# Performance work log

Hardware: AMD Instinct MI355X
Metric: run time of the kernel (lower is better)

Reference implementation:

```python
import jax, jax.numpy as jnp
import numpy as np

B, MAX_OBJS, D = 8, 12, 512
NUM_OBJ, NUM_ACT, NUM_TRS = 37, 6, 3
EMBED = 128
NUM_AA = 100
NUM_CLASSES = 300
ACT_THRES = 0.5
K = MAX_OBJS * NUM_ACT            # 72 candidate (object, action) slots
FINAL_DIM = 2 * (D + 2 * EMBED)   # 1536
# All ordered pairs (i, j), i != j, in lexicographic order. itertools.permutations
# over a sorted index subset is exactly the valid-masked subsequence of this list.
_pairs = np.array([(i, j) for i in range(K) for j in range(K) if i != j], dtype=np.int64)
PAIR_I = jnp.asarray(_pairs[:, 0])
PAIR_J = jnp.asarray(_pairs[:, 1])
P = _pairs.shape[0]               # K*(K-1) = 5112 (static max num pairs)


def setup_inputs() -> dict:
    key = jax.random.key(0)
    ks = jax.random.split(key, 12)
    inp = jax.random.normal(ks[0], (B, MAX_OBJS, D), jnp.float32)
    objmask = jnp.ones((B, MAX_OBJS), jnp.float32)
    # -1 marks 'no composite-action target' for that (obj, act) slot
    AAidxs_tgts = jax.random.randint(ks[1], (B, K), -1, NUM_AA)
    TR_tgts = jax.random.uniform(ks[2], (B, K, K, NUM_TRS), jnp.float32)
    obj_act_lookup = jax.random.randint(ks[3], (NUM_OBJ, NUM_ACT), 0, NUM_AA)
    aa_aa_tr_lookup = jax.random.randint(ks[4], (NUM_AA, NUM_AA, NUM_TRS), 0, NUM_CLASSES)
    s = lambda k, shape: (jax.random.normal(k, shape, jnp.float32) * 0.02)
    return {
        'inp': inp, 'objmask': objmask,
        'TR_tgts': TR_tgts,
        'W_obj': s(ks[5], (NUM_OBJ, D)), 'b_obj': jnp.zeros((NUM_OBJ,), jnp.float32),
        'W_act': s(ks[6], (NUM_ACT, D)), 'b_act': jnp.zeros((NUM_ACT,), jnp.float32),
        'W_tr': s(ks[7], (NUM_TRS, FINAL_DIM)), 'b_tr': jnp.zeros((NUM_TRS,), jnp.float32),
        'W_ne': s(ks[8], (NUM_CLASSES, D)), 'b_ne': jnp.zeros((NUM_CLASSES,), jnp.float32),
        'obj_emb': s(ks[9], (NUM_OBJ, EMBED)), 'act_emb': s(ks[10], (NUM_ACT, EMBED)),
        'AAidxs_tgts': AAidxs_tgts,
        'obj_act_lookup': obj_act_lookup,
        'aa_aa_tr_lookup': aa_aa_tr_lookup,
    }


def reference(inp, objmask, TR_tgts, W_obj, b_obj, W_act, b_act, W_tr, b_tr,
              W_ne, b_ne, obj_emb, act_emb, AAidxs_tgts, obj_act_lookup,
              aa_aa_tr_lookup):
    # training branch (is_eval=False); obj_act_lookup only used in eval branch
    exp_objmask = jnp.repeat(objmask, NUM_ACT, axis=1)                # [B,K]
    masked = inp * objmask[:, :, None]
    pooled = masked.sum(axis=1) / objmask.sum(axis=1, keepdims=True)  # [B,D]
    non_exist_out = pooled @ W_ne.T + b_ne                            # [B,C]
    obj_out = inp @ W_obj.T + b_obj                                   # [B,MO,NO]
    act_out = inp @ W_act.T + b_act                                   # [B,MO,NA]

    posb_action_idxs = jnp.tile(jnp.arange(NUM_ACT), (B, MAX_OBJS))   # [B,K]
    pred_obj_idxs = jnp.repeat(jnp.argmax(obj_out, axis=-1), NUM_ACT, axis=1)  # [B,K]
    posb_inputs = jnp.repeat(inp, NUM_ACT, axis=1)                    # [B,K,D]

    pred_act = (jax.nn.sigmoid(act_out.reshape(B, K)) > ACT_THRES).astype(jnp.float32)
    pred_act = pred_act * exp_objmask
    selected = (pred_act == 1.0) & (AAidxs_tgts != -1)                # [B,K]
    aaidx = jnp.where(selected, AAidxs_tgts, -1)

    posb_obj_emb = obj_emb[pred_obj_idxs]                             # [B,K,E]
    posb_act_emb = act_emb[posb_action_idxs]                          # [B,K,E]
    comp = jnp.concatenate([posb_inputs, posb_obj_emb, posb_act_emb], axis=-1)  # [B,K,FINAL/2]

    # pack valid pairs to the front (stable sort preserves lexicographic order,
    # matching itertools.permutations over the sorted selected index set)
    valid = selected[:, PAIR_I] & selected[:, PAIR_J]                 # [B,P]
    order = jnp.argsort(~valid, axis=1, stable=True)                  # [B,P]
    valid_p = jnp.take_along_axis(valid, order, axis=1)
    i_p = jnp.take_along_axis(jnp.broadcast_to(PAIR_I, (B, P)), order, axis=1)
    j_p = jnp.take_along_axis(jnp.broadcast_to(PAIR_J, (B, P)), order, axis=1)
    b_ix = jnp.arange(B)[:, None]

    pair_out = jnp.where(valid_p[..., None],
                         jnp.concatenate([comp[b_ix, i_p], comp[b_ix, j_p]], axis=-1),
                         -1.0)                                        # [B,P,FINAL_DIM]
    pair_logits = pair_out @ W_tr.T + b_tr                            # [B,P,3]

    aai = aaidx[b_ix, i_p]
    aaj = aaidx[b_ix, j_p]
    ca = aa_aa_tr_lookup[jnp.maximum(aai, 0), jnp.maximum(aaj, 0)]    # [B,P,3]
    ca = jnp.where(valid_p[..., None], ca, -1)
    tr_targets = jnp.where(valid_p[..., None], TR_tgts[b_ix, i_p, j_p], -1.0)

    # diag(logit) @ one_hot(ca) then masked max over pairs == segment max per class
    flat_logit = pair_logits.reshape(B, P * NUM_TRS)
    flat_ca = ca.reshape(B, P * NUM_TRS)
    flat_valid = jnp.repeat(valid_p, NUM_TRS, axis=1)
    seg = jnp.where(flat_valid, flat_ca, NUM_CLASSES)                 # dump invalid to extra segment
    seg_max = jax.vmap(lambda l, s: jax.ops.segment_max(l, s, num_segments=NUM_CLASSES + 1))(
        flat_logit, seg)[:, :NUM_CLASSES]                             # [B,C]
    counts = jax.vmap(lambda s: jax.ops.segment_sum(jnp.ones_like(s), s, num_segments=NUM_CLASSES + 1))(
        seg)[:, :NUM_CLASSES]
    exist = counts > 0
    final_outputs = jnp.where(exist, seg_max, non_exist_out)          # [B,C]

    return final_outputs, pair_logits, tr_targets, act_out, obj_out
```

## Files before the change

kernel.cpp:

```cpp
#include <hip/hip_runtime.h>
#include <hip/hip_bf16.h>

#define Bn    8
#define MO    12
#define Dd    512
#define NOBJ  37
#define NACT  6
#define NTRS  3
#define EMB   128
#define NAA   100
#define NCLS  300
#define Kk    72
#define Pp    5112
#define HALF  768
#define FD    1536

#define OUT_FINAL 0
#define OUT_PLOG  (Bn*NCLS)
#define OUT_TTGT  (OUT_PLOG + Bn*Pp*NTRS)
#define OUT_ACT   (OUT_TTGT + Bn*Pp*NTRS)
#define OUT_OBJ   (OUT_ACT + Bn*Kk)

#define WS_LINP 0
#define WS_EO   (WS_LINP + Bn*MO*6)
#define WS_EA   (WS_EO + NOBJ*6)
#define WS_INV  (WS_EA + NACT*6)
#define WS_NE   (WS_INV + 6)
#define WS_SEG  (WS_NE + Bn*NCLS)
#define WS_PRED (WS_SEG + Bn*NCLS)
#define WS_SEL  (WS_PRED + Bn*MO)
#define WS_AAI  (WS_SEL + Bn*Kk)

__device__ __forceinline__ unsigned fmap(float f) {
  unsigned u = __float_as_uint(f);
  return (u & 0x80000000u) ? ~u : (u | 0x80000000u);
}
__device__ __forceinline__ float funmap(unsigned u) {
  return __uint_as_float((u & 0x80000000u) ? (u & 0x7fffffffu) : ~u);
}

__device__ __forceinline__ float wreduce(float v) {
#pragma unroll
  for (int off = 32; off > 0; off >>= 1) v += __shfl_xor(v, off, 64);
  return v;
}

__device__ __forceinline__ float dotW(const float* __restrict__ wrow,
                                      float4 x0, float4 x1, int lane) {
  const float4* w4 = (const float4*)wrow;
  float4 w0 = w4[lane], w1 = w4[lane + 64];
  float s0 = fmaf(w0.x, x0.x, fmaf(w0.y, x0.y, fmaf(w0.z, x0.z, w0.w * x0.w)));
  float s1 = fmaf(w1.x, x1.x, fmaf(w1.y, x1.y, fmaf(w1.z, x1.z, w1.w * x1.w)));
  return wreduce(s0 + s1);
}

__device__ __forceinline__ float dot512_wave(const float* __restrict__ a,
                                             const float* __restrict__ b, int lane) {
  const float4* b4 = (const float4*)b;
  return dotW(a, b4[lane], b4[lane + 64], lane);
}

__device__ __forceinline__ float dot128_wave(const float* __restrict__ a,
                                             const float* __restrict__ b, int lane) {
  const float2* a2 = (const float2*)a;
  const float2* b2 = (const float2*)b;
  float2 x = a2[lane], y = b2[lane];
  return wreduce(fmaf(x.x, y.x, x.y * y.y));
}

#define W_TOBJ  (Bn*MO)
#define W_TACT  (W_TOBJ + Bn*MO)
#define W_TLINP (W_TACT + Bn*MO*6)
#define W_TEO   (W_TLINP + NOBJ*6)
#define W_TEA   (W_TEO + NACT*6)
#define W_TINV  (W_TEA + NTRS)
#define W_TNE   (W_TINV + Bn*NCLS)
#define W_TOT   (W_TNE + 38)

__global__ __launch_bounds__(256) void k1(
    const float* __restrict__ inp, const float* __restrict__ objmask,
    const float* __restrict__ W_obj, const float* __restrict__ b_obj,
    const float* __restrict__ W_act, const float* __restrict__ b_act,
    const float* __restrict__ W_tr, const float* __restrict__ b_tr,
    const float* __restrict__ W_ne, const float* __restrict__ b_ne,
    const float* __restrict__ obj_emb, const float* __restrict__ act_emb,
    const int* __restrict__ AA,
    float* __restrict__ out, float* __restrict__ ws)
{
  int gt = blockIdx.x * 256 + threadIdx.x;
  int w = gt >> 6, lane = gt & 63;

  if (w < W_TOBJ) {
    int b = w / MO, o = w % MO;
    const float4* x4 = (const float4*)(inp + (b*MO + o)*Dd);
    float4 x0 = x4[lane], x1 = x4[lane + 64];
    float myval = 0.f, best = 0.f;
    int bi = 0;
    for (int c = 0; c < NOBJ; ++c) {
      float s = dotW(W_obj + c*Dd, x0, x1, lane) + b_obj[c];
      if (lane == c) myval = s;
      if (c == 0 || s > best) { best = s; bi = c; }
    }
    if (lane < NOBJ) out[OUT_OBJ + (b*MO + o)*NOBJ + lane] = myval;
    if (lane == 0) ((int*)ws)[WS_PRED + b*MO + o] = bi;
  } else if (w < W_TACT) {
    int r = w - W_TOBJ, b = r / MO, o = r % MO;
    const float4* x4 = (const float4*)(inp + (b*MO + o)*Dd);
    float4 x0 = x4[lane], x1 = x4[lane + 64];
    float myv = 0.f;
    for (int a = 0; a < NACT; ++a) {
      float s = dotW(W_act + a*Dd, x0, x1, lane) + b_act[a];
      if (lane == a) myv = s;
    }
    if (lane < NACT) {
      int k = o*NACT + lane;
      out[OUT_ACT + b*Kk + k] = myv;
      int aa = AA[b*Kk + k];
      int sel = (myv > 0.f) && (objmask[b*MO + o] == 1.0f) && (aa != -1);
      ((int*)ws)[WS_SEL + b*Kk + k] = sel;
      ((int*)ws)[WS_AAI + b*Kk + k] = sel ? aa : -1;
    }
  } else if (w < W_TLINP) {
    int r = w - W_TACT, b = r / (MO*6), r2 = r % (MO*6), o = r2 / 6, th = r2 % 6;
    int t = th >> 1, h = th & 1;
    float v = dot512_wave(W_tr + t*FD + h*HALF, inp + (b*MO + o)*Dd, lane);
    if (!lane) ws[WS_LINP + (b*MO + o)*6 + th] = v;
  } else if (w < W_TEO) {
    int r = w - W_TLINP, oc = r / 6, th = r % 6, t = th >> 1, h = th & 1;
    float v = dot128_wave(W_tr + t*FD + h*HALF + Dd, obj_emb + oc*EMB, lane);
    if (!lane) ws[WS_EO + oc*6 + th] = v;
  } else if (w < W_TEA) {
    int r = w - W_TEO, a = r / 6, th = r % 6, t = th >> 1, h = th & 1;
    float v = dot128_wave(W_tr + t*FD + h*HALF + Dd + EMB, act_emb + a*EMB, lane);
    if (!lane) ws[WS_EA + a*6 + th] = v;
  } else if (w < W_TINV) {
    int t = w - W_TEA;
    const float4* w4 = (const float4*)(W_tr + t*FD);
    float s = 0.f;
#pragma unroll
    for (int i = 0; i < 6; ++i) { float4 x = w4[lane + 64*i]; s += x.x + x.y + x.z + x.w; }
    s = wreduce(s);
    if (!lane) ws[WS_INV + t] = b_tr[t] - s;
  } else if (w < W_TNE) {
    int r = w - W_TINV, b = r / NCLS, c = r % NCLS;
    const float4* i4 = (const float4*)inp;
    float msum = 0.f;
    float4 p0 = make_float4(0.f, 0.f, 0.f, 0.f), p1 = p0;
#pragma unroll
    for (int o = 0; o < MO; ++o) {
      float m = objmask[b*MO + o];
      msum += m;
      float4 v0 = i4[(b*MO + o)*128 + lane];
      float4 v1 = i4[(b*MO + o)*128 + lane + 64];
      p0.x = fmaf(m, v0.x, p0.x); p0.y = fmaf(m, v0.y, p0.y);
      p0.z = fmaf(m, v0.z, p0.z); p0.w = fmaf(m, v0.w, p0.w);
      p1.x = fmaf(m, v1.x, p1.x); p1.y = fmaf(m, v1.y, p1.y);
      p1.z = fmaf(m, v1.z, p1.z); p1.w = fmaf(m, v1.w, p1.w);
    }
    float v = dotW(W_ne + c*Dd, p0, p1, lane) / msum + b_ne[c];
    if (!lane) ws[WS_NE + b*NCLS + c] = v;
  } else if (w < W_TOT) {
    int idx = (w - W_TNE)*64 + lane;
    if (idx < Bn*NCLS) ((unsigned*)ws)[WS_SEG + idx] = 0u;
  }
}

#define NSLICE 20

__global__ __launch_bounds__(256) void k2(
    const float* __restrict__ TRt, const float* __restrict__ b_tr,
    const int* __restrict__ aalut,
    float* __restrict__ out, float* __restrict__ ws)
{
  __shared__ float s_L[Kk*6];
  __shared__ float s_inv[NTRS];
  __shared__ int s_sel[Kk], s_aa[Kk], s_C[Kk], s_T;

  int b = blockIdx.x / NSLICE, slice = blockIdx.x % NSLICE;
  int tid = threadIdx.x;

  if (tid < Kk) {
    s_sel[tid] = ((const int*)ws)[WS_SEL + b*Kk + tid];
    s_aa[tid]  = ((const int*)ws)[WS_AAI + b*Kk + tid];
  } else if (tid < Kk + NTRS) {
    s_inv[tid - Kk] = ws[WS_INV + (tid - Kk)];
  }
  for (int m = tid; m < Kk*6; m += 256) {
    int k = m / 6, th = m % 6, t = th >> 1, h = th & 1;
    int o = k / NACT, a = k % NACT;
    int po = ((const int*)ws)[WS_PRED + b*MO + o];
    float v = ws[WS_LINP + (b*MO + o)*6 + th] + ws[WS_EO + po*6 + th] + ws[WS_EA + a*6 + th];
    if (h == 0) v += b_tr[t];
    s_L[m] = v;
  }
  __syncthreads();
  if (tid == 0) {
    int c = 0;
    for (int k = 0; k < Kk; ++k) { s_C[k] = c; c += s_sel[k]; }
    s_T = c;
  }
  __syncthreads();

  int T = s_T, Vtot = T*(T-1);
  int q = slice*256 + tid;
  if (q < Pp) {
    float* plog = out + OUT_PLOG + (size_t)b*Pp*NTRS;
    float* ttgt = out + OUT_TTGT + (size_t)b*Pp*NTRS;
    int i = q / (Kk-1);
    int jj = q - i*(Kk-1);
    int j = jj + (jj >= i ? 1 : 0);
    int si = s_sel[i], sj = s_sel[j];
    int vb = s_C[i]*(T-1) + (si ? (s_C[j] - (i < j ? 1 : 0)) : 0);
    bool valid = si && sj;
    int pos = valid ? vb : (Vtot + q - vb);
    float l0, l1, l2;
    if (valid) {
      l0 = s_L[i*6+0] + s_L[j*6+1];
      l1 = s_L[i*6+2] + s_L[j*6+3];
      l2 = s_L[i*6+4] + s_L[j*6+5];
    } else { l0 = s_inv[0]; l1 = s_inv[1]; l2 = s_inv[2]; }
    int ob = pos*3;
    plog[ob+0] = l0; plog[ob+1] = l1; plog[ob+2] = l2;
    if (valid) {
      const float* tr = TRt + (((size_t)b*Kk + i)*Kk + j)*NTRS;
      ttgt[ob+0] = tr[0]; ttgt[ob+1] = tr[1]; ttgt[ob+2] = tr[2];
      int base = (s_aa[i]*NAA + s_aa[j])*NTRS;
      unsigned* seg = (unsigned*)ws + WS_SEG + b*NCLS;
      atomicMax(&seg[aalut[base+0]], fmap(l0));
      atomicMax(&seg[aalut[base+1]], fmap(l1));
      atomicMax(&seg[aalut[base+2]], fmap(l2));
    } else {
      ttgt[ob+0] = -1.f; ttgt[ob+1] = -1.f; ttgt[ob+2] = -1.f;
    }
  }
}

__global__ __launch_bounds__(320) void k3(float* __restrict__ out,
                                          const float* __restrict__ ws)
{
  int b = blockIdx.x, c = threadIdx.x;
  if (c < NCLS) {
    unsigned u = ((const unsigned*)ws)[WS_SEG + b*NCLS + c];
    out[OUT_FINAL + b*NCLS + c] = u ? funmap(u) : ws[WS_NE + b*NCLS + c];
  }
}

extern "C" void kernel_launch(void* const* d_in, const int* in_sizes, int n_in,
                              void* d_out, int out_size, void* d_ws, size_t ws_size,
                              hipStream_t stream) {
  (void)in_sizes; (void)n_in; (void)ws_size; (void)out_size;
  const float* inp      = (const float*)d_in[0];
  const float* objmask  = (const float*)d_in[1];
  const float* TRt      = (const float*)d_in[2];
  const float* W_obj    = (const float*)d_in[3];
  const float* b_obj    = (const float*)d_in[4];
  const float* W_act    = (const float*)d_in[5];
  const float* b_act    = (const float*)d_in[6];
  const float* W_tr     = (const float*)d_in[7];
  const float* b_tr     = (const float*)d_in[8];
  const float* W_ne     = (const float*)d_in[9];
  const float* b_ne     = (const float*)d_in[10];
  const float* obj_emb  = (const float*)d_in[11];
  const float* act_emb  = (const float*)d_in[12];
  const int*   AA       = (const int*)d_in[13];
  const int*   aalut    = (const int*)d_in[15];
  float* out = (float*)d_out;
  float* ws  = (float*)d_ws;

  hipLaunchKernelGGL(k1, dim3((W_TOT + 3) / 4), dim3(256), 0, stream,
                     inp, objmask, W_obj, b_obj, W_act, b_act, W_tr, b_tr,
                     W_ne, b_ne, obj_emb, act_emb, AA, out, ws);
  hipLaunchKernelGGL(k2, dim3(Bn * NSLICE), dim3(256), 0, stream,
                     TRt, b_tr, aalut, out, ws);
  hipLaunchKernelGGL(k3, dim3(Bn), dim3(320), 0, stream, out, ws);
}
```

Before: 102.2 us.

## Spread obj/act logits across waves and fold finalize kernel into k2 via last-block counter

```diff
diff --git a/kernel.cpp b/kernel.cpp
--- a/kernel.cpp
+++ b/kernel.cpp
@@ -25,11 +25,12 @@
 #define WS_EO   (WS_LINP + Bn*MO*6)
 #define WS_EA   (WS_EO + NOBJ*6)
 #define WS_INV  (WS_EA + NACT*6)
-#define WS_NE   (WS_INV + 6)
-#define WS_SEG  (WS_NE + Bn*NCLS)
-#define WS_PRED (WS_SEG + Bn*NCLS)
-#define WS_SEL  (WS_PRED + Bn*MO)
-#define WS_AAI  (WS_SEL + Bn*Kk)
+#define WS_NE   840
+#define WS_OBJ  (WS_NE + Bn*NCLS)
+#define WS_ACT  (WS_OBJ + Bn*MO*NOBJ)
+#define WS_SEG  (WS_ACT + Bn*Kk)
+#define WS_CNT  (WS_SEG + Bn*NCLS)
+#define NZERO   (Bn*NCLS + Bn)
 
 __device__ __forceinline__ unsigned fmap(float f) {
   unsigned u = __float_as_uint(f);
@@ -68,14 +69,14 @@
   return wreduce(fmaf(x.x, y.x, x.y * y.y));
 }
 
-#define W_TOBJ  (Bn*MO)
-#define W_TACT  (W_TOBJ + Bn*MO)
-#define W_TLINP (W_TACT + Bn*MO*6)
-#define W_TEO   (W_TLINP + NOBJ*6)
-#define W_TEA   (W_TEO + NACT*6)
-#define W_TINV  (W_TEA + NTRS)
-#define W_TNE   (W_TINV + Bn*NCLS)
-#define W_TOT   (W_TNE + 38)
+#define W_OBJ_E  (Bn*MO*NOBJ)
+#define W_ACT_E  (W_OBJ_E + Bn*Kk)
+#define W_LINP_E (W_ACT_E + Bn*MO*6)
+#define W_EO_E   (W_LINP_E + NOBJ*6)
+#define W_EA_E   (W_EO_E + NACT*6)
+#define W_INV_E  (W_EA_E + NTRS)
+#define W_NE_E   (W_INV_E + Bn*NCLS)
+#define W_TOT    (W_NE_E + 38)
 
 __global__ __launch_bounds__(256) void k1(
     const float* __restrict__ inp, const float* __restrict__ objmask,
@@ -84,65 +85,44 @@
     const float* __restrict__ W_tr, const float* __restrict__ b_tr,
     const float* __restrict__ W_ne, const float* __restrict__ b_ne,
     const float* __restrict__ obj_emb, const float* __restrict__ act_emb,
-    const int* __restrict__ AA,
     float* __restrict__ out, float* __restrict__ ws)
 {
   int gt = blockIdx.x * 256 + threadIdx.x;
   int w = gt >> 6, lane = gt & 63;
 
-  if (w < W_TOBJ) {
-    int b = w / MO, o = w % MO;
-    const float4* x4 = (const float4*)(inp + (b*MO + o)*Dd);
-    float4 x0 = x4[lane], x1 = x4[lane + 64];
-    float myval = 0.f, best = 0.f;
-    int bi = 0;
-    for (int c = 0; c < NOBJ; ++c) {
-      float s = dotW(W_obj + c*Dd, x0, x1, lane) + b_obj[c];
-      if (lane == c) myval = s;
-      if (c == 0 || s > best) { best = s; bi = c; }
-    }
-    if (lane < NOBJ) out[OUT_OBJ + (b*MO + o)*NOBJ + lane] = myval;
-    if (lane == 0) ((int*)ws)[WS_PRED + b*MO + o] = bi;
-  } else if (w < W_TACT) {
-    int r = w - W_TOBJ, b = r / MO, o = r % MO;
-    const float4* x4 = (const float4*)(inp + (b*MO + o)*Dd);
-    float4 x0 = x4[lane], x1 = x4[lane + 64];
-    float myv = 0.f;
-    for (int a = 0; a < NACT; ++a) {
-      float s = dotW(W_act + a*Dd, x0, x1, lane) + b_act[a];
-      if (lane == a) myv = s;
-    }
-    if (lane < NACT) {
-      int k = o*NACT + lane;
-      out[OUT_ACT + b*Kk + k] = myv;
-      int aa = AA[b*Kk + k];
-      int sel = (myv > 0.f) && (objmask[b*MO + o] == 1.0f) && (aa != -1);
-      ((int*)ws)[WS_SEL + b*Kk + k] = sel;
-      ((int*)ws)[WS_AAI + b*Kk + k] = sel ? aa : -1;
-    }
-  } else if (w < W_TLINP) {
-    int r = w - W_TACT, b = r / (MO*6), r2 = r % (MO*6), o = r2 / 6, th = r2 % 6;
+  if (w < W_OBJ_E) {
+    int b = w / (MO*NOBJ), r = w % (MO*NOBJ), o = r / NOBJ, c = r % NOBJ;
+    float v = dot512_wave(W_obj + c*Dd, inp + (b*MO + o)*Dd, lane) + b_obj[c];
+    if (!lane) { out[OUT_OBJ + (b*MO + o)*NOBJ + c] = v; ws[WS_OBJ + (b*MO + o)*NOBJ + c] = v; }
+  } else if (w < W_ACT_E) {
+    int r = w - W_OBJ_E, b = r / Kk, k = r % Kk, o = k / NACT, a = k % NACT;
+    float v = dot512_wave(W_act + a*Dd, inp + (b*MO + o)*Dd, lane) + b_act[a];
+    if (!lane) { out[OUT_ACT + b*Kk + k] = v; ws[WS_ACT + b*Kk + k] = v; }
+  } else if (w < W_LINP_E) {
+    int r = w - W_ACT_E, b = r / (MO*6), r2 = r % (MO*6), o = r2 / 6, th = r2 % 6;
     int t = th >> 1, h = th & 1;
     float v = dot512_wave(W_tr + t*FD + h*HALF, inp + (b*MO + o)*Dd, lane);
     if (!lane) ws[WS_LINP + (b*MO + o)*6 + th] = v;
-  } else if (w < W_TEO) {
-    int r = w - W_TLINP, oc = r / 6, th = r % 6, t = th >> 1, h = th & 1;
+  } else if (w < W_EO_E) {
+    int r = w - W_LINP_E, oc = r / 6, th = r % 6, t = th >> 1, h = th & 1;
     float v = dot128_wave(W_tr + t*FD + h*HALF + Dd, obj_emb + oc*EMB, lane);
     if (!lane) ws[WS_EO + oc*6 + th] = v;
-  } else if (w < W_TEA) {
-    int r = w - W_TEO, a = r / 6, th = r % 6, t = th >> 1, h = th & 1;
-    float v = dot128_wave(W_tr + t*FD + h*HALF + Dd + EMB, act_emb + a*EMB, lane);
-    if (!lane) ws[WS_EA + a*6 + th] = v;
-  } else if (w < W_TINV) {
-    int t = w - W_TEA;
-    const float4* w4 = (const float4*)(W_tr + t*FD);
-    float s = 0.f;
+  } else if (w < W_INV_E) {
+    if (w < W_EA_E) {
+      int r = w - W_EO_E, a = r / 6, th = r % 6, t = th >> 1, h = th & 1;
+      float v = dot128_wave(W_tr + t*FD + h*HALF + Dd + EMB, act_emb + a*EMB, lane);
+      if (!lane) ws[WS_EA + a*6 + th] = v;
+    } else {
+      int t = w - W_EA_E;
+      const float4* w4 = (const float4*)(W_tr + t*FD);
+      float s = 0.f;
 #pragma unroll
-    for (int i = 0; i < 6; ++i) { float4 x = w4[lane + 64*i]; s += x.x + x.y + x.z + x.w; }
-    s = wreduce(s);
-    if (!lane) ws[WS_INV + t] = b_tr[t] - s;
-  } else if (w < W_TNE) {
-    int r = w - W_TINV, b = r / NCLS, c = r % NCLS;
+      for (int i = 0; i < 6; ++i) { float4 x = w4[lane + 64*i]; s += x.x + x.y + x.z + x.w; }
+      s = wreduce(s);
+      if (!lane) ws[WS_INV + t] = b_tr[t] - s;
+    }
+  } else if (w < W_NE_E) {
+    int r = w - W_INV_E, b = r / NCLS, c = r % NCLS;
     const float4* i4 = (const float4*)inp;
     float msum = 0.f;
     float4 p0 = make_float4(0.f, 0.f, 0.f, 0.f), p1 = p0;
@@ -160,40 +140,49 @@
     float v = dotW(W_ne + c*Dd, p0, p1, lane) / msum + b_ne[c];
     if (!lane) ws[WS_NE + b*NCLS + c] = v;
   } else if (w < W_TOT) {
-    int idx = (w - W_TNE)*64 + lane;
-    if (idx < Bn*NCLS) ((unsigned*)ws)[WS_SEG + idx] = 0u;
+    int idx = (w - W_NE_E)*64 + lane;
+    if (idx < NZERO) ((unsigned*)ws)[WS_SEG + idx] = 0u;
   }
 }
 
 #define NSLICE 20
 
 __global__ __launch_bounds__(256) void k2(
-    const float* __restrict__ TRt, const float* __restrict__ b_tr,
+    const float* __restrict__ objmask, const float* __restrict__ TRt,
+    const float* __restrict__ b_tr, const int* __restrict__ AA,
     const int* __restrict__ aalut,
     float* __restrict__ out, float* __restrict__ ws)
 {
   __shared__ float s_L[Kk*6];
   __shared__ float s_inv[NTRS];
-  __shared__ int s_sel[Kk], s_aa[Kk], s_C[Kk], s_T;
+  __shared__ int s_sel[Kk], s_aa[Kk], s_C[Kk], s_pred[MO], s_T, s_last;
 
   int b = blockIdx.x / NSLICE, slice = blockIdx.x % NSLICE;
   int tid = threadIdx.x;
 
-  if (tid < Kk) {
-    s_sel[tid] = ((const int*)ws)[WS_SEL + b*Kk + tid];
-    s_aa[tid]  = ((const int*)ws)[WS_AAI + b*Kk + tid];
-  } else if (tid < Kk + NTRS) {
-    s_inv[tid - Kk] = ws[WS_INV + (tid - Kk)];
-  }
+  if (tid < MO) {
+    const float* p = ws + WS_OBJ + (b*MO + tid)*NOBJ;
+    float best = p[0]; int bi = 0;
+    for (int c = 1; c < NOBJ; ++c) { float v = p[c]; if (v > best) { best = v; bi = c; } }
+    s_pred[tid] = bi;
+  } else if (tid < MO + NTRS) {
+    s_inv[tid - MO] = ws[WS_INV + (tid - MO)];
+  } else if (tid >= 64 && tid < 64 + Kk) {
+    int k = tid - 64, o = k / NACT;
+    int aa = AA[b*Kk + k];
+    int sel = (ws[WS_ACT + b*Kk + k] > 0.f) && (objmask[b*MO + o] == 1.0f) && (aa != -1);
+    s_sel[k] = sel;
+    s_aa[k] = sel ? aa : -1;
+  }
+  __syncthreads();
   for (int m = tid; m < Kk*6; m += 256) {
     int k = m / 6, th = m % 6, t = th >> 1, h = th & 1;
     int o = k / NACT, a = k % NACT;
-    int po = ((const int*)ws)[WS_PRED + b*MO + o];
-    float v = ws[WS_LINP + (b*MO + o)*6 + th] + ws[WS_EO + po*6 + th] + ws[WS_EA + a*6 + th];
+    float v = ws[WS_LINP + (b*MO + o)*6 + th] + ws[WS_EO + s_pred[o]*6 + th]
+            + ws[WS_EA + a*6 + th];
     if (h == 0) v += b_tr[t];
     s_L[m] = v;
   }
-  __syncthreads();
   if (tid == 0) {
     int c = 0;
     for (int k = 0; k < Kk; ++k) { s_C[k] = c; c += s_sel[k]; }
@@ -233,15 +222,20 @@
       ttgt[ob+0] = -1.f; ttgt[ob+1] = -1.f; ttgt[ob+2] = -1.f;
     }
   }
-}
-
-__global__ __launch_bounds__(320) void k3(float* __restrict__ out,
-                                          const float* __restrict__ ws)
-{
-  int b = blockIdx.x, c = threadIdx.x;
-  if (c < NCLS) {
-    unsigned u = ((const unsigned*)ws)[WS_SEG + b*NCLS + c];
-    out[OUT_FINAL + b*NCLS + c] = u ? funmap(u) : ws[WS_NE + b*NCLS + c];
+
+  __threadfence();
+  __syncthreads();
+  if (tid == 0) {
+    unsigned old = atomicAdd((unsigned*)ws + WS_CNT + b, 1u);
+    s_last = (old == NSLICE - 1);
+  }
+  __syncthreads();
+  if (s_last) {
+    __threadfence();
+    for (int c = tid; c < NCLS; c += 256) {
+      unsigned u = atomicMax((unsigned*)ws + WS_SEG + b*NCLS + c, 0u);
+      out[OUT_FINAL + b*NCLS + c] = u ? funmap(u) : ws[WS_NE + b*NCLS + c];
+    }
   }
 }
 
@@ -269,8 +263,7 @@
 
   hipLaunchKernelGGL(k1, dim3((W_TOT + 3) / 4), dim3(256), 0, stream,
                      inp, objmask, W_obj, b_obj, W_act, b_act, W_tr, b_tr,
-                     W_ne, b_ne, obj_emb, act_emb, AA, out, ws);
+                     W_ne, b_ne, obj_emb, act_emb, out, ws);
   hipLaunchKernelGGL(k2, dim3(Bn * NSLICE), dim3(256), 0, stream,
-                     TRt, b_tr, aalut, out, ws);
-  hipLaunchKernelGGL(k3, dim3(Bn), dim3(320), 0, stream, out, ws);
-}
+                     objmask, TRt, b_tr, AA, aalut, out, ws);
+}
```

New measurement: 109.7 us. 1.07x slower.
